# Performance work log

Hardware: AMD Instinct MI355X
Metric: run time of the kernel (lower is better)

The kernel has to match this reference:

```python
import jax, jax.numpy as jnp
import numpy as np

H, D_NOPE, D_ROPE, D_V, L_KV, HID = 16, 128, 64, 128, 512, 2048
D_QK = D_NOPE + D_ROPE
THETA = 10000.0
EPS = 1e-6


def _rope(x, positions):
    # neox-style rotary over last dim (D_ROPE); x: [T, ..., D_ROPE]
    half = D_ROPE // 2
    inv_freq = 1.0 / (THETA ** (jnp.arange(half, dtype=jnp.float32) * 2.0 / D_ROPE))
    ang = positions.astype(jnp.float32)[:, None] * inv_freq[None, :]  # [T, half]
    shape = (x.shape[0],) + (1,) * (x.ndim - 2) + (half,)
    cos, sin = jnp.cos(ang).reshape(shape), jnp.sin(ang).reshape(shape)
    x1, x2 = x[..., :half], x[..., half:]
    return jnp.concatenate([x1 * cos - x2 * sin, x2 * cos + x1 * sin], axis=-1)


def _rmsnorm(x, w):
    var = jnp.mean(x * x, axis=-1, keepdims=True)
    return x * jax.lax.rsqrt(var + EPS) * w


def setup_inputs() -> dict:
    key = jax.random.key(0)
    ks = jax.random.split(key, 6)
    T = 4096
    s = lambda fan_in: 1.0 / np.sqrt(fan_in)
    return {
        "positions": jnp.arange(T, dtype=jnp.int32),
        "hidden_states": jax.random.normal(ks[0], (T, HID), jnp.float32),
        "Wq": jax.random.normal(ks[1], (HID, H * D_QK), jnp.float32) * s(HID),
        "Wkva": jax.random.normal(ks[2], (HID, L_KV + D_ROPE), jnp.float32) * s(HID),
        "kv_a_ln_w": jnp.ones((L_KV,), jnp.float32),
        "Wkvb": jax.random.normal(ks[3], (L_KV, H * (D_NOPE + D_V)), jnp.float32) * s(L_KV),
        "Wo": jax.random.normal(ks[4], (H * D_V, HID), jnp.float32) * s(H * D_V),
    }


def reference(positions, hidden_states, Wq, Wkva, kv_a_ln_w, Wkvb, Wo):
    T = hidden_states.shape[0]
    scaling = 1.0 / np.sqrt(D_QK)

    q = (hidden_states @ Wq).reshape(T, H, D_QK)
    q_nope, q_pe = q[..., :D_NOPE], q[..., D_NOPE:]

    latent = hidden_states @ Wkva                    # [T, L_KV + D_ROPE]
    kv_a = _rmsnorm(latent[:, :L_KV], kv_a_ln_w)     # [T, L_KV]
    k_pe = latent[:, L_KV:]                          # [T, D_ROPE] (shared across heads)

    kv = (kv_a @ Wkvb).reshape(T, H, D_NOPE + D_V)
    k_nope, v = kv[..., :D_NOPE], kv[..., D_NOPE:]

    q_pe = _rope(q_pe, positions)                    # [T, H, D_ROPE]
    k_pe = _rope(k_pe, positions)                    # [T, D_ROPE]

    q = jnp.concatenate([q_nope, q_pe], axis=-1)     # [T, H, D_QK]
    k = jnp.concatenate(
        [k_nope, jnp.broadcast_to(k_pe[:, None, :], (T, H, D_ROPE))], axis=-1)

    scores = jnp.einsum("thd,shd->hts", q, k) * scaling        # [H, T, T]
    causal = positions[:, None] >= positions[None, :]           # [T, T]
    scores = jnp.where(causal[None], scores, jnp.finfo(scores.dtype).min)
    attn = jax.nn.softmax(scores, axis=-1)
    out = jnp.einsum("hts,shd->thd", attn, v)                   # [T, H, D_V]
    return out.reshape(T, H * D_V) @ Wo                          # [T, HID]
```

## Files before the change

kernel.cpp:

```cpp
#include <hip/hip_runtime.h>
#include <hip/hip_bf16.h>

#define T_LEN 4096
#define HID_DIM 2048
#define NH 16
#define DNOPE 128
#define DROPE 64
#define DV 128
#define LKV 512
#define DQK 192

#define BN 64

typedef __attribute__((ext_vector_type(8))) __bf16 bf16x8;
typedef __attribute__((ext_vector_type(4))) float f32x4;
typedef __attribute__((ext_vector_type(4))) short s16x4;

__device__ __forceinline__ unsigned short f2b(float f) {
  unsigned u = __builtin_bit_cast(unsigned, f);
  unsigned r = (u + 0x7FFFu + ((u >> 16) & 1u)) >> 16;
  return (unsigned short)r;
}

#define GL2LDS16(gp, lp)                                                   \
  __builtin_amdgcn_global_load_lds(                                        \
      (const __attribute__((address_space(1))) unsigned int*)(gp),         \
      (__attribute__((address_space(3))) unsigned int*)(lp), 16, 0, 0)

#if __has_builtin(__builtin_amdgcn_mfma_f32_16x16x16bf16_1k)
#define HAVE_MFMA16 1
__device__ __forceinline__ f32x4 mfma16(s16x4 a, s16x4 b, f32x4 c) {
  return __builtin_amdgcn_mfma_f32_16x16x16bf16_1k(a, b, c, 0, 0, 0);
}
#elif __has_builtin(__builtin_amdgcn_mfma_f32_16x16x16_bf16)
#define HAVE_MFMA16 1
typedef __attribute__((ext_vector_type(4))) __bf16 bf16x4v;
__device__ __forceinline__ f32x4 mfma16(s16x4 a, s16x4 b, f32x4 c) {
  return __builtin_amdgcn_mfma_f32_16x16x16_bf16(
      __builtin_bit_cast(bf16x4v, a), __builtin_bit_cast(bf16x4v, b), c, 0, 0, 0);
}
#else
#define HAVE_MFMA16 0
#endif

__global__ void k_cvt(const float* __restrict__ in, unsigned short* __restrict__ out, int n) {
  int i = blockIdx.x * 256 + threadIdx.x;
  if (i < n) out[i] = f2b(in[i]);
}

__global__ void k_transpose_all(const float* __restrict__ Wq, const float* __restrict__ Wkva,
                                const float* __restrict__ Wkvb, const float* __restrict__ Wo,
                                unsigned short* __restrict__ WqT, unsigned short* __restrict__ WkvaT,
                                unsigned short* __restrict__ WkvbT, unsigned short* __restrict__ WoT) {
  __shared__ float t[32][33];
  int bid = blockIdx.x;
  const float* in; unsigned short* out; int R, C, bx, by;
  if (bid < 6144)      { in = Wq;   out = WqT;   R = 2048; C = 3072; bx = bid % 96;  by = bid / 96; }
  else if (bid < 7296) { int b = bid - 6144; in = Wkva; out = WkvaT; R = 2048; C = 576;  bx = b % 18;  by = b / 18; }
  else if (bid < 9344) { int b = bid - 7296; in = Wkvb; out = WkvbT; R = 512;  C = 4096; bx = b % 128; by = b / 128; }
  else                 { int b = bid - 9344; in = Wo;   out = WoT;   R = 2048; C = 2048; bx = b % 64;  by = b / 64; }
  int c0 = bx * 32, r0 = by * 32;
  int tx = threadIdx.x, ty = threadIdx.y;
#pragma unroll
  for (int k = 0; k < 4; k++)
    t[ty + 8 * k][tx] = in[(size_t)(r0 + ty + 8 * k) * C + c0 + tx];
  __syncthreads();
#pragma unroll
  for (int k = 0; k < 4; k++)
    out[(size_t)(c0 + ty + 8 * k) * R + r0 + tx] = f2b(t[tx][ty + 8 * k]);
}

#define GEMM_CORE(Aptr, Btptr, Nn, Kk, ldaa, ldbb)                                         \
  __shared__ unsigned short As[128 * 32];                                                  \
  __shared__ unsigned short Bs[128 * 32];                                                  \
  int tid = threadIdx.x;                                                                   \
  int lane = tid & 63, w = tid >> 6;                                                       \
  int quad = lane >> 4, l16 = lane & 15;                                                   \
  int wm = (w >> 1) * 64, wn = (w & 1) * 64;                                               \
  int i0 = tid, i1 = tid + 256;                                                            \
  int rA0 = i0 >> 2, rA1 = i1 >> 2;                                                       \
  int c80 = (i0 & 3) * 8, c81 = (i1 & 3) * 8;                                              \
  const unsigned short* Ag0 = (Aptr) + (size_t)(m0 + rA0) * (ldaa) + c80;                  \
  const unsigned short* Ag1 = (Aptr) + (size_t)(m0 + rA1) * (ldaa) + c81;                  \
  int bR0 = n0 + rA0; if (bR0 >= (Nn)) bR0 = (Nn) - 1;                                     \
  int bR1 = n0 + rA1; if (bR1 >= (Nn)) bR1 = (Nn) - 1;                                     \
  const unsigned short* Bg0 = (Btptr) + (size_t)bR0 * (ldbb) + c80;                        \
  const unsigned short* Bg1 = (Btptr) + (size_t)bR1 * (ldbb) + c81;                        \
  f32x4 acc[4][4] = {};                                                                    \
  for (int k0 = 0; k0 < (Kk); k0 += 32) {                                                  \
    GL2LDS16(Ag0 + k0, &As[i0 * 8]);                                                       \
    GL2LDS16(Ag1 + k0, &As[i1 * 8]);                                                       \
    GL2LDS16(Bg0 + k0, &Bs[i0 * 8]);                                                       \
    GL2LDS16(Bg1 + k0, &Bs[i1 * 8]);                                                       \
    __syncthreads();                                                                       \
    bf16x8 aF[4], bF[4];                                                                   \
    _Pragma("unroll")                                                                      \
    for (int i = 0; i < 4; i++)                                                            \
      aF[i] = *(const bf16x8*)&As[(wm + i * 16 + l16) * 32 + quad * 8];                    \
    _Pragma("unroll")                                                                      \
    for (int j = 0; j < 4; j++)                                                            \
      bF[j] = *(const bf16x8*)&Bs[(wn + j * 16 + l16) * 32 + quad * 8];                    \
    _Pragma("unroll")                                                                      \
    for (int i = 0; i < 4; i++)                                                            \
      _Pragma("unroll")                                                                    \
      for (int j = 0; j < 4; j++)                                                          \
        acc[i][j] = __builtin_amdgcn_mfma_f32_16x16x32_bf16(aF[i], bF[j], acc[i][j], 0, 0, 0); \
    __syncthreads();                                                                       \
  }                                                                                        \
  int row0 = m0 + wm + quad * 4; (void)row0;

__global__ __launch_bounds__(256) void k_gemm128(
    const unsigned short* __restrict__ A, const unsigned short* __restrict__ Bt,
    float* __restrict__ Cf, int N, int K, int lda, int ldb, int ldc) {
  int m0 = blockIdx.y * 128, n0 = blockIdx.x * 128;
  GEMM_CORE(A, Bt, N, K, lda, ldb)
#pragma unroll
  for (int i = 0; i < 4; i++)
#pragma unroll
    for (int j = 0; j < 4; j++) {
      int col = n0 + wn + j * 16 + l16;
      if (col < N)
#pragma unroll
        for (int r = 0; r < 4; r++)
          Cf[(size_t)(row0 + i * 16 + r) * ldc + col] = acc[i][j][r];
    }
}

__global__ __launch_bounds__(256) void k_gemm_proj(
    const unsigned short* __restrict__ A, const unsigned short* __restrict__ WqT,
    const unsigned short* __restrict__ WkvaT, const int* __restrict__ pos,
    unsigned short* __restrict__ Qh, float* __restrict__ latentf) {
  int bxx = blockIdx.x;
  bool iswq = bxx < 24;
  const unsigned short* Bt = iswq ? WqT : WkvaT;
  int N = iswq ? NH * DQK : (LKV + DROPE);
  int m0 = blockIdx.y * 128, n0 = (iswq ? bxx : bxx - 24) * 128;
  GEMM_CORE(A, Bt, N, HID_DIM, HID_DIM, HID_DIM)
  if (iswq) {
    const float scale = 0.07216878364870323f;
    int b64 = (n0 + wn) >> 6;
    int h = b64 / 3, rem3 = b64 - 3 * h;
    unsigned short* Qb = Qh + (size_t)h * T_LEN * DQK;
    if (rem3 < 2) {
#pragma unroll
      for (int i = 0; i < 4; i++)
#pragma unroll
        for (int r = 0; r < 4; r++) {
          int t = row0 + i * 16 + r;
#pragma unroll
          for (int j = 0; j < 4; j++)
            Qb[(size_t)t * DQK + rem3 * 64 + j * 16 + l16] = f2b(acc[i][j][r] * scale);
        }
    } else {
#pragma unroll
      for (int i = 0; i < 4; i++)
#pragma unroll
        for (int r = 0; r < 4; r++) {
          int t = row0 + i * 16 + r;
          float p = (float)pos[t];
#pragma unroll
          for (int j = 0; j < 2; j++) {
            int idx = j * 16 + l16;
            float inv = __expf((float)idx * -0.2878231366242557f);
            float sn, cs;
            __sincosf(p * inv, &sn, &cs);
            float x1 = acc[i][j][r] * scale, x2 = acc[i][j + 2][r] * scale;
            Qb[(size_t)t * DQK + DNOPE + idx]      = f2b(x1 * cs - x2 * sn);
            Qb[(size_t)t * DQK + DNOPE + 32 + idx] = f2b(x2 * cs + x1 * sn);
          }
        }
    }
  } else {
#pragma unroll
    for (int i = 0; i < 4; i++)
#pragma unroll
      for (int j = 0; j < 4; j++) {
        int col = n0 + wn + j * 16 + l16;
        if (col < LKV + DROPE)
#pragma unroll
          for (int r = 0; r < 4; r++)
            latentf[(size_t)(row0 + i * 16 + r) * (LKV + DROPE) + col] = acc[i][j][r];
      }
  }
}

__global__ __launch_bounds__(256) void k_gemm_wkvb(
    const unsigned short* __restrict__ A, const unsigned short* __restrict__ Bt,
    unsigned short* __restrict__ Kh, unsigned short* __restrict__ VT) {
  int m0 = blockIdx.y * 128, n0 = blockIdx.x * 128;
  GEMM_CORE(A, Bt, NH * 256, LKV, LKV, LKV)
#pragma unroll
  for (int i = 0; i < 4; i++)
#pragma unroll
    for (int j = 0; j < 4; j++) {
      int col = n0 + wn + j * 16 + l16;
      int h = col >> 8, c = col & 255;
      int t0 = row0 + i * 16;
      if (c < 128) {
#pragma unroll
        for (int r = 0; r < 4; r++)
          Kh[((size_t)h * T_LEN + t0 + r) * DQK + c] = f2b(acc[i][j][r]);
      } else {
        unsigned lo = (unsigned)f2b(acc[i][j][0]) | ((unsigned)f2b(acc[i][j][1]) << 16);
        unsigned hi = (unsigned)f2b(acc[i][j][2]) | ((unsigned)f2b(acc[i][j][3]) << 16);
        uint2 pk = {lo, hi};
        *(uint2*)&VT[(size_t)(h * 128 + c - 128) * T_LEN + t0] = pk;
      }
    }
}

__global__ __launch_bounds__(256) void k_prep_latent(
    const float* __restrict__ latent, const float* __restrict__ w,
    const int* __restrict__ pos,
    unsigned short* __restrict__ kva, unsigned short* __restrict__ Kh) {
  __shared__ float red[256];
  int t = blockIdx.x;
  const float* row = latent + (size_t)t * (LKV + DROPE);
  float ss = 0.f;
  for (int c = threadIdx.x; c < LKV; c += 256) { float v = row[c]; ss += v * v; }
  red[threadIdx.x] = ss;
  __syncthreads();
  for (int s = 128; s > 0; s >>= 1) {
    if (threadIdx.x < s) red[threadIdx.x] += red[threadIdx.x + s];
    __syncthreads();
  }
  float rs = rsqrtf(red[0] / (float)LKV + 1e-6f);
  for (int c = threadIdx.x; c < LKV; c += 256)
    kva[(size_t)t * LKV + c] = f2b(row[c] * rs * w[c]);
  if (threadIdx.x < DROPE) {
    int i = threadIdx.x;
    float p = (float)pos[t];
    float val;
    if (i < 32) {
      float x1 = row[LKV + i], x2 = row[LKV + i + 32];
      float inv = __expf(-(float)i * 0.2878231366242557f);
      float sn, cs; __sincosf(p * inv, &sn, &cs);
      val = x1 * cs - x2 * sn;
    } else {
      float x1 = row[LKV + i - 32], x2 = row[LKV + i];
      float inv = __expf(-(float)(i - 32) * 0.2878231366242557f);
      float sn, cs; __sincosf(p * inv, &sn, &cs);
      val = x2 * cs + x1 * sn;
    }
    unsigned short vb = f2b(val);
#pragma unroll
    for (int h = 0; h < NH; h++)
      Kh[((size_t)h * T_LEN + t) * DQK + DNOPE + i] = vb;
  }
}

__global__ __launch_bounds__(256, 2) void k_flash(
    const unsigned short* __restrict__ Qh, const unsigned short* __restrict__ Kh,
    const unsigned short* __restrict__ VT, unsigned short* __restrict__ attn) {
  int bx = blockIdx.x;
  int h = bx & 15;
  int t = (bx & 255) >> 4;
  int qb = (bx < 256) ? (31 - t) : t;
  int m0 = qb * 128;
  int diagA = 2 * qb, diagB = 2 * qb + 1;
  int NT = 2 * qb + 2;

  __shared__ unsigned short Ks[2 * 64 * 24 * 8];
  __shared__ unsigned short Vs[2 * 128 * 8 * 8];

  int tid = threadIdx.x, lane = tid & 63, w = tid >> 6;
  int quad = lane >> 4, l16 = lane & 15;
  int x = l16 & 7;

  const unsigned short* Qbase = Qh + (size_t)h * T_LEN * DQK;
  const unsigned short* Kbase = Kh + (size_t)h * T_LEN * DQK;
  const unsigned short* Vbase = VT + (size_t)h * DV * T_LEN;

  bf16x8 qfS[6], qfL[6];
#pragma unroll
  for (int kk = 0; kk < 6; kk++) {
    qfS[kk] = *(const bf16x8*)(Qbase + (size_t)(m0 + w * 16 + l16) * DQK + kk * 32 + quad * 8);
    qfL[kk] = *(const bf16x8*)(Qbase + (size_t)(m0 + 64 + w * 16 + l16) * DQK + kk * 32 + quad * 8);
  }

  int koff[6], voff[4];
#pragma unroll
  for (int k = 0; k < 6; k++) {
    int c = tid + k * 256;
    int row = c / 24, sc = c - row * 24;
    int cg = (sc & 0x18) | ((sc ^ row) & 7);
    koff[k] = row * DQK + cg * 8;
  }
#pragma unroll
  for (int k = 0; k < 4; k++) {
    int c = tid + k * 256;
    int row = c >> 3, sc = c & 7;
    int cg = sc ^ (row & 7);
    voff[k] = row * T_LEN + cg * 8;
  }

  int kEo[4], kOo[4], vAo[4];
#pragma unroll
  for (int st = 0; st < 4; st++) {
    int rb = (st * 16 + l16) * 192;
    kEo[st] = rb + ((quad ^ x) * 8);
    kOo[st] = rb + (((quad + 4) ^ x) * 8);
    vAo[st] = l16 * 64 + (((st * 2 + (quad >> 1)) ^ x) * 8) + (quad & 1) * 4;
  }

  f32x4 OaccS[8] = {}, OaccL[8] = {};
  float liS = 0.f, liL = 0.f;
  int mS = m0 + w * 16 + l16;
  int mL = mS + 64;

#if !HAVE_MFMA16
  int lA = l16 + ((quad & 1) << 5);
  int lB = lA + 16;
  bool lowq = (quad < 2);
  int vFo[2];
#pragma unroll
  for (int u = 0; u < 2; u++)
    vFo[u] = l16 * 64 + (((u * 4 + quad) ^ x) * 8);
#endif

#define STAGE(buf)                                                                         \
  do {                                                                                     \
    unsigned short* ksd = Ks + (buf) * (64 * 24 * 8);                                      \
    unsigned short* vsd = Vs + (buf) * (128 * 8 * 8);                                      \
    _Pragma("unroll")                                                                      \
    for (int k = 0; k < 6; k++) GL2LDS16(Kbase + koff[k], &ksd[(tid + k * 256) * 8]);      \
    _Pragma("unroll")                                                                      \
    for (int k = 0; k < 4; k++) GL2LDS16(Vbase + voff[k], &vsd[(tid + k * 256) * 8]);      \
    _Pragma("unroll")                                                                      \
    for (int k = 0; k < 6; k++) koff[k] += BN * DQK;                                       \
    _Pragma("unroll")                                                                      \
    for (int k = 0; k < 4; k++) voff[k] += BN;                                             \
  } while (0)

#define PIPE_BARRIER()                                                                     \
  do {                                                                                     \
    asm volatile("s_waitcnt vmcnt(0)" ::: "memory");                                       \
    __builtin_amdgcn_s_barrier();                                                          \
    __builtin_amdgcn_sched_barrier(0);                                                     \
  } while (0)

  STAGE(0);
  PIPE_BARRIER();

  int cur = 0;
  for (int j = 0; j < NT; ++j) {
    if (j + 1 < NT) STAGE(cur ^ 1);

    const unsigned short* KsB = Ks + cur * (64 * 24 * 8);
    const unsigned short* VsB = Vs + cur * (128 * 8 * 8);

    f32x4 ScS[4] = {}, ScL[4] = {};
#pragma unroll
    for (int kk = 0; kk < 6; kk++) {
#pragma unroll
      for (int st = 0; st < 4; st++) {
        bf16x8 kb = *(const bf16x8*)(KsB + ((kk & 1) ? kOo[st] : kEo[st]) + (kk >> 1) * 64);
        ScS[st] = __builtin_amdgcn_mfma_f32_16x16x32_bf16(kb, qfS[kk], ScS[st], 0, 0, 0);
        ScL[st] = __builtin_amdgcn_mfma_f32_16x16x32_bf16(kb, qfL[kk], ScL[st], 0, 0, 0);
      }
    }

    int n0 = j * BN;
    if (j >= diagA) {
#pragma unroll
      for (int st = 0; st < 4; st++)
#pragma unroll
        for (int r = 0; r < 4; r++) {
          int s = n0 + st * 16 + quad * 4 + r;
          if (s > mS) ScS[st][r] = -1e30f;
        }
    }
    if (j == diagB) {
#pragma unroll
      for (int st = 0; st < 4; st++)
#pragma unroll
        for (int r = 0; r < 4; r++) {
          int s = n0 + st * 16 + quad * 4 + r;
          if (s > mL) ScL[st][r] = -1e30f;
        }
    }

    unsigned p0S[4], p1S[4], p0L[4], p1L[4];
#pragma unroll
    for (int st = 0; st < 4; st++) {
      float e0 = __expf(ScS[st][0]);
      float e1 = __expf(ScS[st][1]);
      float e2 = __expf(ScS[st][2]);
      float e3 = __expf(ScS[st][3]);
      liS += (e0 + e1) + (e2 + e3);
      p0S[st] = __builtin_amdgcn_perm(__builtin_bit_cast(unsigned, e1),
                                      __builtin_bit_cast(unsigned, e0), 0x07060302u);
      p1S[st] = __builtin_amdgcn_perm(__builtin_bit_cast(unsigned, e3),
                                      __builtin_bit_cast(unsigned, e2), 0x07060302u);
      float f0 = __expf(ScL[st][0]);
      float f1 = __expf(ScL[st][1]);
      float f2 = __expf(ScL[st][2]);
      float f3 = __expf(ScL[st][3]);
      liL += (f0 + f1) + (f2 + f3);
      p0L[st] = __builtin_amdgcn_perm(__builtin_bit_cast(unsigned, f1),
                                      __builtin_bit_cast(unsigned, f0), 0x07060302u);
      p1L[st] = __builtin_amdgcn_perm(__builtin_bit_cast(unsigned, f3),
                                      __builtin_bit_cast(unsigned, f2), 0x07060302u);
    }

#if HAVE_MFMA16
#pragma unroll
    for (int st = 0; st < 4; st++) {
      uint2 puS; puS.x = p0S[st]; puS.y = p1S[st];
      s16x4 pbS = __builtin_bit_cast(s16x4, puS);
      uint2 puL; puL.x = p0L[st]; puL.y = p1L[st];
      s16x4 pbL = __builtin_bit_cast(s16x4, puL);
#pragma unroll
      for (int dt = 0; dt < 8; dt++) {
        s16x4 va = __builtin_bit_cast(s16x4, *(const uint2*)(VsB + vAo[st] + dt * 1024));
        OaccS[dt] = mfma16(va, pbS, OaccS[dt]);
        OaccL[dt] = mfma16(va, pbL, OaccL[dt]);
      }
    }
#else
#pragma unroll
    for (int u = 0; u < 2; u++) {
      int a0 = __shfl((int)p0S[2 * u], lA, 64);
      int a1 = __shfl((int)p0S[2 * u + 1], lA, 64);
      int b0 = __shfl((int)p1S[2 * u], lA, 64);
      int b1 = __shfl((int)p1S[2 * u + 1], lA, 64);
      int c0 = __shfl((int)p0S[2 * u], lB, 64);
      int c1 = __shfl((int)p0S[2 * u + 1], lB, 64);
      int d0 = __shfl((int)p1S[2 * u], lB, 64);
      int d1 = __shfl((int)p1S[2 * u + 1], lB, 64);
      int4 pkS;
      pkS.x = lowq ? a0 : a1; pkS.y = lowq ? b0 : b1;
      pkS.z = lowq ? c0 : c1; pkS.w = lowq ? d0 : d1;
      bf16x8 pbS = __builtin_bit_cast(bf16x8, pkS);
      int sa0 = __shfl((int)p0L[2 * u], lA, 64);
      int sa1 = __shfl((int)p0L[2 * u + 1], lA, 64);
      int sb0 = __shfl((int)p1L[2 * u], lA, 64);
      int sb1 = __shfl((int)p1L[2 * u + 1], lA, 64);
      int sc0 = __shfl((int)p0L[2 * u], lB, 64);
      int sc1 = __shfl((int)p0L[2 * u + 1], lB, 64);
      int sd0 = __shfl((int)p1L[2 * u], lB, 64);
      int sd1 = __shfl((int)p1L[2 * u + 1], lB, 64);
      int4 pkL;
      pkL.x = lowq ? sa0 : sa1; pkL.y = lowq ? sb0 : sb1;
      pkL.z = lowq ? sc0 : sc1; pkL.w = lowq ? sd0 : sd1;
      bf16x8 pbL = __builtin_bit_cast(bf16x8, pkL);
#pragma unroll
      for (int dt = 0; dt < 8; dt++) {
        bf16x8 va = *(const bf16x8*)(VsB + vFo[u] + dt * 1024);
        OaccS[dt] = __builtin_amdgcn_mfma_f32_16x16x32_bf16(va, pbS, OaccS[dt], 0, 0, 0);
        OaccL[dt] = __builtin_amdgcn_mfma_f32_16x16x32_bf16(va, pbL, OaccL[dt], 0, 0, 0);
      }
    }
#endif

    PIPE_BARRIER();
    cur ^= 1;
  }

  liS += __shfl_xor(liS, 16, 64);
  liS += __shfl_xor(liS, 32, 64);
  liL += __shfl_xor(liL, 16, 64);
  liL += __shfl_xor(liL, 32, 64);

  float invS = 1.f / liS;
  float invL = 1.f / liL;
  unsigned short* dstS = attn + (size_t)mS * HID_DIM + h * DV + quad * 4;
  unsigned short* dstL = attn + (size_t)mL * HID_DIM + h * DV + quad * 4;
#pragma unroll
  for (int dt = 0; dt < 8; dt++) {
    unsigned lo = (unsigned)f2b(OaccS[dt][0] * invS) |
                  ((unsigned)f2b(OaccS[dt][1] * invS) << 16);
    unsigned hi = (unsigned)f2b(OaccS[dt][2] * invS) |
                  ((unsigned)f2b(OaccS[dt][3] * invS) << 16);
    uint2 pkv = {lo, hi};
    *(uint2*)(dstS + dt * 16) = pkv;
    unsigned lo2 = (unsigned)f2b(OaccL[dt][0] * invL) |
                   ((unsigned)f2b(OaccL[dt][1] * invL) << 16);
    unsigned hi2 = (unsigned)f2b(OaccL[dt][2] * invL) |
                   ((unsigned)f2b(OaccL[dt][3] * invL) << 16);
    uint2 pkv2 = {lo2, hi2};
    *(uint2*)(dstL + dt * 16) = pkv2;
  }
#undef STAGE
#undef PIPE_BARRIER
}

extern "C" void kernel_launch(void* const* d_in, const int* in_sizes, int n_in,
                              void* d_out, int out_size, void* d_ws, size_t ws_size,
                              hipStream_t stream) {
  const int*   positions = (const int*)d_in[0];
  const float* hs   = (const float*)d_in[1];
  const float* Wq   = (const float*)d_in[2];
  const float* Wkva = (const float*)d_in[3];
  const float* lnw  = (const float*)d_in[4];
  const float* Wkvb = (const float*)d_in[5];
  const float* Wo   = (const float*)d_in[6];
  float* out = (float*)d_out;

  char* p = (char*)d_ws;
  size_t off = 0;
  auto alloc = [&](size_t bytes) {
    char* r = p + off;
    off = (off + bytes + 255) & ~(size_t)255;
    return r;
  };
  unsigned short* hsb     = (unsigned short*)alloc((size_t)T_LEN * HID_DIM * 2);
  unsigned short* WqT     = (unsigned short*)alloc((size_t)(NH * DQK) * HID_DIM * 2);
  unsigned short* WkvaT   = (unsigned short*)alloc((size_t)(LKV + DROPE) * HID_DIM * 2);
  unsigned short* WkvbT   = (unsigned short*)alloc((size_t)(NH * 256) * LKV * 2);
  unsigned short* WoT     = (unsigned short*)alloc((size_t)HID_DIM * HID_DIM * 2);
  unsigned short* Qh      = (unsigned short*)alloc((size_t)NH * T_LEN * DQK * 2);
  unsigned short* kva     = (unsigned short*)alloc((size_t)T_LEN * LKV * 2);
  unsigned short* Kh      = (unsigned short*)alloc((size_t)NH * T_LEN * DQK * 2);
  unsigned short* VT      = (unsigned short*)alloc((size_t)NH * DV * T_LEN * 2);
  unsigned short* attn    = (unsigned short*)alloc((size_t)T_LEN * HID_DIM * 2);
  float*          latentf = (float*)alloc((size_t)T_LEN * (LKV + DROPE) * 4);

  k_cvt<<<(T_LEN * HID_DIM + 255) / 256, 256, 0, stream>>>(hs, hsb, T_LEN * HID_DIM);
  k_transpose_all<<<13440, dim3(32, 8), 0, stream>>>(Wq, Wkva, Wkvb, Wo, WqT, WkvaT, WkvbT, WoT);

  k_gemm_proj<<<dim3(29, T_LEN / 128), 256, 0, stream>>>(hsb, WqT, WkvaT, positions, Qh, latentf);

  k_prep_latent<<<T_LEN, 256, 0, stream>>>(latentf, lnw, positions, kva, Kh);

  k_gemm_wkvb<<<dim3((NH * 256) / 128, T_LEN / 128), 256, 0, stream>>>(kva, WkvbT, Kh, VT);

  k_flash<<<dim3(512), 256, 0, stream>>>(Qh, Kh, VT, attn);

  k_gemm128<<<dim3(HID_DIM / 128, T_LEN / 128), 256, 0, stream>>>(
      attn, WoT, out, HID_DIM, HID_DIM, HID_DIM, HID_DIM, HID_DIM);
}
```

Baseline: 479.7 us.

## Fuse hidden-state cast into transpose, swizzle GEMM blocks across XCDs, warp-level RMSNorm

The standalone fp32-to-bf16 cast kernel is folded into the weight transpose launch as extra vectorized blocks, which removes one kernel launch and widens the memory accesses. The three GEMM kernels remap block indices so that neighbouring tiles land on the same XCD, aiming for better L2 reuse. The latent prep kernel now handles one token per wavefront, using vector loads and shuffle reductions instead of a shared-memory tree reduction, and launches a quarter as many blocks. These are small, independent changes to memory traffic and launch overhead. The swizzle assumes the grid size divides evenly by eight.

```diff
diff --git a/kernel.cpp b/kernel.cpp
--- a/kernel.cpp
+++ b/kernel.cpp
@@ -43,24 +43,42 @@
 #define HAVE_MFMA16 0
 #endif
 
-__global__ void k_cvt(const float* __restrict__ in, unsigned short* __restrict__ out, int n) {
-  int i = blockIdx.x * 256 + threadIdx.x;
-  if (i < n) out[i] = f2b(in[i]);
+__device__ __forceinline__ void xcd_swz(int nbx, int* bx, int* by) {
+  int lin = blockIdx.y * nbx + blockIdx.x;
+  int cpx = (nbx * gridDim.y) >> 3;
+  int swz = (lin & 7) * cpx + (lin >> 3);
+  *bx = swz % nbx;
+  *by = swz / nbx;
 }
 
 __global__ void k_transpose_all(const float* __restrict__ Wq, const float* __restrict__ Wkva,
                                 const float* __restrict__ Wkvb, const float* __restrict__ Wo,
+                                const float* __restrict__ hs,
                                 unsigned short* __restrict__ WqT, unsigned short* __restrict__ WkvaT,
-                                unsigned short* __restrict__ WkvbT, unsigned short* __restrict__ WoT) {
+                                unsigned short* __restrict__ WkvbT, unsigned short* __restrict__ WoT,
+                                unsigned short* __restrict__ hsb) {
+  int bid = blockIdx.x;
+  int tx = threadIdx.x, ty = threadIdx.y;
+  if (bid >= 13440) {
+    int i = (bid - 13440) * 256 + ty * 32 + tx;
+    const float4* in4 = (const float4*)hs;
+    float4 v0 = in4[i * 2];
+    float4 v1 = in4[i * 2 + 1];
+    unsigned a = (unsigned)f2b(v0.x) | ((unsigned)f2b(v0.y) << 16);
+    unsigned b = (unsigned)f2b(v0.z) | ((unsigned)f2b(v0.w) << 16);
+    unsigned c = (unsigned)f2b(v1.x) | ((unsigned)f2b(v1.y) << 16);
+    unsigned d = (unsigned)f2b(v1.z) | ((unsigned)f2b(v1.w) << 16);
+    uint4 pk = {a, b, c, d};
+    ((uint4*)hsb)[i] = pk;
+    return;
+  }
   __shared__ float t[32][33];
-  int bid = blockIdx.x;
   const float* in; unsigned short* out; int R, C, bx, by;
   if (bid < 6144)      { in = Wq;   out = WqT;   R = 2048; C = 3072; bx = bid % 96;  by = bid / 96; }
   else if (bid < 7296) { int b = bid - 6144; in = Wkva; out = WkvaT; R = 2048; C = 576;  bx = b % 18;  by = b / 18; }
   else if (bid < 9344) { int b = bid - 7296; in = Wkvb; out = WkvbT; R = 512;  C = 4096; bx = b % 128; by = b / 128; }
   else                 { int b = bid - 9344; in = Wo;   out = WoT;   R = 2048; C = 2048; bx = b % 64;  by = b / 64; }
   int c0 = bx * 32, r0 = by * 32;
-  int tx = threadIdx.x, ty = threadIdx.y;
 #pragma unroll
   for (int k = 0; k < 4; k++)
     t[ty + 8 * k][tx] = in[(size_t)(r0 + ty + 8 * k) * C + c0 + tx];
@@ -78,7 +96,7 @@
   int quad = lane >> 4, l16 = lane & 15;                                                   \
   int wm = (w >> 1) * 64, wn = (w & 1) * 64;                                               \
   int i0 = tid, i1 = tid + 256;                                                            \
-  int rA0 = i0 >> 2, rA1 = i1 >> 2;                                                       \
+  int rA0 = i0 >> 2, rA1 = i1 >> 2;                                                        \
   int c80 = (i0 & 3) * 8, c81 = (i1 & 3) * 8;                                              \
   const unsigned short* Ag0 = (Aptr) + (size_t)(m0 + rA0) * (ldaa) + c80;                  \
   const unsigned short* Ag1 = (Aptr) + (size_t)(m0 + rA1) * (ldaa) + c81;                  \
@@ -112,7 +130,8 @@
 __global__ __launch_bounds__(256) void k_gemm128(
     const unsigned short* __restrict__ A, const unsigned short* __restrict__ Bt,
     float* __restrict__ Cf, int N, int K, int lda, int ldb, int ldc) {
-  int m0 = blockIdx.y * 128, n0 = blockIdx.x * 128;
+  int bxs, bys; xcd_swz(gridDim.x, &bxs, &bys);
+  int m0 = bys * 128, n0 = bxs * 128;
   GEMM_CORE(A, Bt, N, K, lda, ldb)
 #pragma unroll
   for (int i = 0; i < 4; i++)
@@ -130,11 +149,11 @@
     const unsigned short* __restrict__ A, const unsigned short* __restrict__ WqT,
     const unsigned short* __restrict__ WkvaT, const int* __restrict__ pos,
     unsigned short* __restrict__ Qh, float* __restrict__ latentf) {
-  int bxx = blockIdx.x;
+  int bxx, byy; xcd_swz(gridDim.x, &bxx, &byy);
   bool iswq = bxx < 24;
   const unsigned short* Bt = iswq ? WqT : WkvaT;
   int N = iswq ? NH * DQK : (LKV + DROPE);
-  int m0 = blockIdx.y * 128, n0 = (iswq ? bxx : bxx - 24) * 128;
+  int m0 = byy * 128, n0 = (iswq ? bxx : bxx - 24) * 128;
   GEMM_CORE(A, Bt, N, HID_DIM, HID_DIM, HID_DIM)
   if (iswq) {
     const float scale = 0.07216878364870323f;
@@ -187,7 +206,8 @@
 __global__ __launch_bounds__(256) void k_gemm_wkvb(
     const unsigned short* __restrict__ A, const unsigned short* __restrict__ Bt,
     unsigned short* __restrict__ Kh, unsigned short* __restrict__ VT) {
-  int m0 = blockIdx.y * 128, n0 = blockIdx.x * 128;
+  int bxs, bys; xcd_swz(gridDim.x, &bxs, &bys);
+  int m0 = bys * 128, n0 = bxs * 128;
   GEMM_CORE(A, Bt, NH * 256, LKV, LKV, LKV)
 #pragma unroll
   for (int i = 0; i < 4; i++)
@@ -213,40 +233,47 @@
     const float* __restrict__ latent, const float* __restrict__ w,
     const int* __restrict__ pos,
     unsigned short* __restrict__ kva, unsigned short* __restrict__ Kh) {
-  __shared__ float red[256];
-  int t = blockIdx.x;
+  int t = blockIdx.x * 4 + (threadIdx.x >> 6);
+  int lane = threadIdx.x & 63;
   const float* row = latent + (size_t)t * (LKV + DROPE);
-  float ss = 0.f;
-  for (int c = threadIdx.x; c < LKV; c += 256) { float v = row[c]; ss += v * v; }
-  red[threadIdx.x] = ss;
-  __syncthreads();
-  for (int s = 128; s > 0; s >>= 1) {
-    if (threadIdx.x < s) red[threadIdx.x] += red[threadIdx.x + s];
-    __syncthreads();
-  }
-  float rs = rsqrtf(red[0] / (float)LKV + 1e-6f);
-  for (int c = threadIdx.x; c < LKV; c += 256)
-    kva[(size_t)t * LKV + c] = f2b(row[c] * rs * w[c]);
-  if (threadIdx.x < DROPE) {
-    int i = threadIdx.x;
-    float p = (float)pos[t];
-    float val;
-    if (i < 32) {
-      float x1 = row[LKV + i], x2 = row[LKV + i + 32];
-      float inv = __expf(-(float)i * 0.2878231366242557f);
-      float sn, cs; __sincosf(p * inv, &sn, &cs);
-      val = x1 * cs - x2 * sn;
-    } else {
-      float x1 = row[LKV + i - 32], x2 = row[LKV + i];
-      float inv = __expf(-(float)(i - 32) * 0.2878231366242557f);
-      float sn, cs; __sincosf(p * inv, &sn, &cs);
-      val = x2 * cs + x1 * sn;
-    }
-    unsigned short vb = f2b(val);
-#pragma unroll
-    for (int h = 0; h < NH; h++)
-      Kh[((size_t)h * T_LEN + t) * DQK + DNOPE + i] = vb;
-  }
+  f32x4 a = *(const f32x4*)&row[lane * 8];
+  f32x4 b = *(const f32x4*)&row[lane * 8 + 4];
+  float ss = a[0] * a[0] + a[1] * a[1] + a[2] * a[2] + a[3] * a[3] +
+             b[0] * b[0] + b[1] * b[1] + b[2] * b[2] + b[3] * b[3];
+  ss += __shfl_xor(ss, 1, 64);
+  ss += __shfl_xor(ss, 2, 64);
+  ss += __shfl_xor(ss, 4, 64);
+  ss += __shfl_xor(ss, 8, 64);
+  ss += __shfl_xor(ss, 16, 64);
+  ss += __shfl_xor(ss, 32, 64);
+  float rs = rsqrtf(ss / (float)LKV + 1e-6f);
+  f32x4 w0 = *(const f32x4*)&w[lane * 8];
+  f32x4 w1 = *(const f32x4*)&w[lane * 8 + 4];
+  unsigned q0 = (unsigned)f2b(a[0] * rs * w0[0]) | ((unsigned)f2b(a[1] * rs * w0[1]) << 16);
+  unsigned q1 = (unsigned)f2b(a[2] * rs * w0[2]) | ((unsigned)f2b(a[3] * rs * w0[3]) << 16);
+  unsigned q2 = (unsigned)f2b(b[0] * rs * w1[0]) | ((unsigned)f2b(b[1] * rs * w1[1]) << 16);
+  unsigned q3 = (unsigned)f2b(b[2] * rs * w1[2]) | ((unsigned)f2b(b[3] * rs * w1[3]) << 16);
+  uint4 pk = {q0, q1, q2, q3};
+  *(uint4*)&kva[(size_t)t * LKV + lane * 8] = pk;
+
+  int i = lane;
+  float p = (float)pos[t];
+  float val;
+  if (i < 32) {
+    float x1 = row[LKV + i], x2 = row[LKV + i + 32];
+    float inv = __expf(-(float)i * 0.2878231366242557f);
+    float sn, cs; __sincosf(p * inv, &sn, &cs);
+    val = x1 * cs - x2 * sn;
+  } else {
+    float x1 = row[LKV + i - 32], x2 = row[LKV + i];
+    float inv = __expf(-(float)(i - 32) * 0.2878231366242557f);
+    float sn, cs; __sincosf(p * inv, &sn, &cs);
+    val = x2 * cs + x1 * sn;
+  }
+  unsigned short vb = f2b(val);
+#pragma unroll
+  for (int h = 0; h < NH; h++)
+    Kh[((size_t)h * T_LEN + t) * DQK + DNOPE + i] = vb;
 }
 
 __global__ __launch_bounds__(256, 2) void k_flash(
@@ -516,12 +543,12 @@
   unsigned short* attn    = (unsigned short*)alloc((size_t)T_LEN * HID_DIM * 2);
   float*          latentf = (float*)alloc((size_t)T_LEN * (LKV + DROPE) * 4);
 
-  k_cvt<<<(T_LEN * HID_DIM + 255) / 256, 256, 0, stream>>>(hs, hsb, T_LEN * HID_DIM);
-  k_transpose_all<<<13440, dim3(32, 8), 0, stream>>>(Wq, Wkva, Wkvb, Wo, WqT, WkvaT, WkvbT, WoT);
+  k_transpose_all<<<17536, dim3(32, 8), 0, stream>>>(Wq, Wkva, Wkvb, Wo, hs,
+                                                     WqT, WkvaT, WkvbT, WoT, hsb);
 
   k_gemm_proj<<<dim3(29, T_LEN / 128), 256, 0, stream>>>(hsb, WqT, WkvaT, positions, Qh, latentf);
 
-  k_prep_latent<<<T_LEN, 256, 0, stream>>>(latentf, lnw, positions, kva, Kh);
+  k_prep_latent<<<T_LEN / 4, 256, 0, stream>>>(latentf, lnw, positions, kva, Kh);
 
   k_gemm_wkvb<<<dim3((NH * 256) / 128, T_LEN / 128), 256, 0, stream>>>(kva, WkvbT, Kh, VT);
 
```

Result: faster. 463.3 us (-3.4%).
